# Kernel optimization log

Hardware: AMD Instinct MI355X
Metric: run time of the kernel (lower is better)

## Reference

```python
import jax, jax.numpy as jnp
import numpy as np

N_QUBITS = 8
DIM = 2 ** N_QUBITS  # 256
BSZ = 32768
N_OPS = 20

# Deterministic stand-in for tq.RandomLayer(n_ops=20): a fixed random list of
# {rx, ry, rz, cnot} ops on random wires, angles supplied via rl_angles.
_rng = np.random.RandomState(0)
_RL_OPS = []
for _i in range(N_OPS):
    _kind = ['rx', 'ry', 'rz', 'cnot'][int(_rng.randint(4))]
    if _kind == 'cnot':
        _w = _rng.choice(N_QUBITS, 2, replace=False)
        _RL_OPS.append((_kind, int(_w[0]), int(_w[1])))
    else:
        _RL_OPS.append((_kind, int(_rng.randint(N_QUBITS)), -1))


def _apply_1q(state, wire, kind, half_angle):
    """Apply a single-qubit rotation to state [bsz, DIM]. wire 0 = MSB."""
    bsz = state.shape[0]
    left = 2 ** wire
    right = DIM // (2 * left)
    st = state.reshape(bsz, left, 2, right)
    ha = jnp.broadcast_to(jnp.asarray(half_angle).reshape(-1), (bsz,))
    c = jnp.cos(ha)[:, None, None]
    s = jnp.sin(ha)[:, None, None]
    s0, s1 = st[:, :, 0, :], st[:, :, 1, :]
    if kind == 'ry':
        n0, n1 = c * s0 - s * s1, s * s0 + c * s1
    elif kind == 'rx':
        n0, n1 = c * s0 - 1j * s * s1, -1j * s * s0 + c * s1
    else:  # rz
        n0, n1 = (c - 1j * s) * s0, (c + 1j * s) * s1
    return jnp.stack([n0, n1], axis=2).reshape(bsz, DIM)


def _apply_cnot(state, control, target):
    bsz = state.shape[0]
    st = state.reshape((bsz,) + (2,) * N_QUBITS)
    c_ax, t_ax = 1 + control, 1 + target
    a = jnp.take(st, 0, axis=c_ax)  # control = 0 block: identity
    b = jnp.take(st, 1, axis=c_ax)  # control = 1 block: X on target
    b = jnp.flip(b, axis=t_ax - (1 if t_ax > c_ax else 0))
    return jnp.stack([a, b], axis=c_ax).reshape(bsz, DIM)


# Precomputed PauliZ sign table: signs[w, k] = +1 if bit w of k is 0 else -1.
_idx = np.arange(DIM)
_bits = (_idx[None, :] >> (N_QUBITS - 1 - np.arange(N_QUBITS)[:, None])) & 1
_SIGNS = jnp.asarray(1.0 - 2.0 * _bits, jnp.float32)  # [N_QUBITS, DIM]


def setup_inputs() -> dict:
    key = jax.random.key(0)
    k1, k2, k3, k4 = jax.random.split(key, 4)
    return {
        'x': jax.random.uniform(k1, (BSZ, N_QUBITS), dtype=jnp.float32),
        'rl_angles': jax.random.normal(k2, (N_OPS,), dtype=jnp.float32),
        'theta_rx': jax.random.normal(k3, (1,), dtype=jnp.float32),
        'theta_ry': jax.random.normal(k4, (1,), dtype=jnp.float32),
    }


def reference(x, rl_angles, theta_rx, theta_ry):
    bsz = x.shape[0]
    # |0...0> initial state
    state = jnp.zeros((bsz, DIM), jnp.complex64).at[:, 0].set(1.0)
    # GeneralEncoder: RY(x_i) on wire i (per-sample angles)
    for i in range(N_QUBITS):
        state = _apply_1q(state, i, 'ry', x[:, i] * 0.5)
    # RandomLayer: 20 fixed random ops
    for k, (kind, w0, w1) in enumerate(_RL_OPS):
        if kind == 'cnot':
            state = _apply_cnot(state, w0, w1)
        else:
            state = _apply_1q(state, w0, kind, rl_angles[k] * 0.5)
    # shared trainable RX then RY on every wire
    for w in range(N_QUBITS):
        state = _apply_1q(state, w, 'rx', theta_rx[0] * 0.5)
        state = _apply_1q(state, w, 'ry', theta_ry[0] * 0.5)
    # MeasureAll(PauliZ): <Z_w> = sum_k |amp_k|^2 * sign(bit_w(k))
    probs = state.real ** 2 + state.imag ** 2  # [bsz, DIM]
    return probs @ _SIGNS.T  # [bsz, N_QUBITS]
```

## Files before the change

### kernel.cpp

```cpp
#include <hip/hip_runtime.h>
#include <stdint.h>

#define NQ 8
#define DIM 256
#define BSZ 32768
#define NOPS 20
#define SPT 2

typedef float v2f __attribute__((ext_vector_type(2)));


struct COps { int kind[NOPS]; int w0[NOPS]; int w1[NOPS]; };

struct CMT {
  uint32_t mt[624]; int pos;
  constexpr CMT(uint32_t seed) : mt{}, pos(624) {
    for (int i = 0; i < 624; ++i) {
      mt[i] = seed;
      seed = 1812433253u * (seed ^ (seed >> 30)) + (uint32_t)(i + 1);
    }
  }
  constexpr uint32_t next32() {
    if (pos >= 624) {
      for (int i = 0; i < 624; ++i) {
        uint32_t y = (mt[i] & 0x80000000u) | (mt[(i + 1) % 624] & 0x7fffffffu);
        mt[i] = mt[(i + 397) % 624] ^ (y >> 1) ^ ((y & 1u) ? 0x9908b0dfu : 0u);
      }
      pos = 0;
    }
    uint32_t y = mt[pos++];
    y ^= y >> 11; y ^= (y << 7) & 0x9d2c5680u; y ^= (y << 15) & 0xefc60000u; y ^= y >> 18;
    return y;
  }
  constexpr uint32_t interval(uint32_t mx) {
    if (mx == 0u) return 0u;
    uint32_t mask = mx;
    mask |= mask >> 1; mask |= mask >> 2; mask |= mask >> 4; mask |= mask >> 8; mask |= mask >> 16;
    uint32_t v = next32() & mask;
    while (v > mx) v = next32() & mask;
    return v;
  }
};

constexpr COps decode_ops() {
  COps o{}; CMT r(0u);
  for (int k = 0; k < NOPS; ++k) {
    const uint32_t kind = r.interval(3u);
    o.kind[k] = (int)kind;
    if (kind == 3u) {
      int perm[NQ] = {0,1,2,3,4,5,6,7};
      for (int i = NQ - 1; i >= 1; --i) {
        const uint32_t j = r.interval((uint32_t)i);
        const int t = perm[i]; perm[i] = perm[(int)j]; perm[(int)j] = t;
      }
      o.w0[k] = perm[0]; o.w1[k] = perm[1];
    } else {
      o.w0[k] = (int)r.interval(7u);
      o.w1[k] = -1;
    }
  }
  return o;
}

constexpr COps OPS = decode_ops();


__device__ __forceinline__ float rfl(float v) {
  return __builtin_bit_cast(float, __builtin_amdgcn_readfirstlane(__builtin_bit_cast(int, v)));
}

template<int MASK>
__device__ __forceinline__ float lanexf(float v) {
  int i = __builtin_bit_cast(int, v);
  int r;
  if constexpr (MASK == 1)      r = __builtin_amdgcn_update_dpp(0, i, 0xB1, 0xF, 0xF, true);
  else if constexpr (MASK == 2) r = __builtin_amdgcn_update_dpp(0, i, 0x4E, 0xF, 0xF, true);
  else if constexpr (MASK == 8) r = __builtin_amdgcn_update_dpp(0, i, 0x128, 0xF, 0xF, true);
  else {
    int h = __builtin_amdgcn_update_dpp(0, i, 0x141, 0xF, 0xF, true);
    r     = __builtin_amdgcn_update_dpp(0, h, 0x1B, 0xF, 0xF, true);
  }
  return __builtin_bit_cast(float, r);
}

template<int MASK>
__device__ __forceinline__ v2f lanex2(v2f v) {
  v2f r; r.x = lanexf<MASK>(v.x); r.y = lanexf<MASK>(v.y); return r;
}

__device__ __forceinline__ v2f vswap(v2f v) { return __builtin_shufflevector(v, v, 1, 0); }
__device__ __forceinline__ v2f vsplat(float s) { v2f r = {s, s}; return r; }


template<int W>
__device__ __forceinline__ void g_rx_t(v2f (&v)[16], int l, float t) {
  constexpr int m = 1 << (7 - W);
  const v2f tpm = {t, -t};
  if constexpr (m >= 16) {
    constexpr int M = m >> 4;
    #pragma unroll
    for (int j0 = 0; j0 < 16; ++j0) if ((j0 & M) == 0) {
      const int j1 = j0 | M;
      v2f a = v[j0], b = v[j1];
      v[j0] = a + tpm * vswap(b);
      v[j1] = b + tpm * vswap(a);
    }
  } else {
    #pragma unroll
    for (int j = 0; j < 16; ++j) {
      v2f x = lanex2<m>(v[j]);
      v[j] = v[j] + tpm * vswap(x);
    }
  }
}

template<int W>
__device__ __forceinline__ void g_ry_t(v2f (&v)[16], int l, float t) {
  constexpr int m = 1 << (7 - W);
  if constexpr (m >= 16) {
    constexpr int M = m >> 4;
    const v2f vtn = vsplat(-t), vtp = vsplat(t);
    #pragma unroll
    for (int j0 = 0; j0 < 16; ++j0) if ((j0 & M) == 0) {
      const int j1 = j0 | M;
      v2f a = v[j0], b = v[j1];
      v[j0] = a + vtn * b;
      v[j1] = b + vtp * a;
    }
  } else {
    const v2f ts = vsplat((l & m) ? t : -t);
    #pragma unroll
    for (int j = 0; j < 16; ++j) {
      v2f x = lanex2<m>(v[j]);
      v[j] = v[j] + ts * x;
    }
  }
}

template<int W>
__device__ __forceinline__ void g_rz_t(v2f (&v)[16], int l, float t) {
  constexpr int m = 1 << (7 - W);
  if constexpr (m >= 16) {
    constexpr int M = m >> 4;
    const v2f tpm = {t, -t};
    #pragma unroll
    for (int j = 0; j < 16; ++j) {
      v2f sw = vswap(v[j]);
      if ((j & M) == 0) v[j] = v[j] + tpm * sw;
      else              v[j] = v[j] - tpm * sw;
    }
  } else {
    const v2f ts = (l & m) ? (v2f){-t, t} : (v2f){t, -t};
    #pragma unroll
    for (int j = 0; j < 16; ++j) v[j] = v[j] + ts * vswap(v[j]);
  }
}

template<int WC, int WT>
__device__ __forceinline__ void g_cnot(v2f (&v)[16], int l) {
  constexpr int mc = 1 << (7 - WC);
  constexpr int mt = 1 << (7 - WT);
  if constexpr (mt >= 16) {
    constexpr int M = mt >> 4;
    if constexpr (mc >= 16) {
      constexpr int MC = mc >> 4;
      #pragma unroll
      for (int j0 = 0; j0 < 16; ++j0) if ((j0 & M) == 0 && (j0 & MC) != 0) {
        const int j1 = j0 | M;
        v2f t = v[j0]; v[j0] = v[j1]; v[j1] = t;
      }
    } else {
      const bool bit = (l & mc) != 0;
      #pragma unroll
      for (int j0 = 0; j0 < 16; ++j0) if ((j0 & M) == 0) {
        const int j1 = j0 | M;
        v2f a = v[j0], b = v[j1];
        v[j0] = bit ? b : a;
        v[j1] = bit ? a : b;
      }
    }
  } else {
    if constexpr (mc >= 16) {
      constexpr int MC = mc >> 4;
      #pragma unroll
      for (int j = 0; j < 16; ++j) if (j & MC) v[j] = lanex2<mt>(v[j]);
    } else if constexpr ((mc == 8 || mc == 4) && mt != 4) {
      constexpr int BM   = (mc == 8) ? 0xC : 0xA;
      constexpr int ctrl = (mt == 1) ? 0xB1 : (mt == 2) ? 0x4E : 0x128;
      #pragma unroll
      for (int j = 0; j < 16; ++j) {
        int ir = __builtin_bit_cast(int, v[j].x);
        int ii = __builtin_bit_cast(int, v[j].y);
        ir = __builtin_amdgcn_update_dpp(ir, ir, ctrl, 0xF, BM, false);
        ii = __builtin_amdgcn_update_dpp(ii, ii, ctrl, 0xF, BM, false);
        v[j].x = __builtin_bit_cast(float, ir);
        v[j].y = __builtin_bit_cast(float, ii);
      }
    } else {
      const bool bit = (l & mc) != 0;
      #pragma unroll
      for (int j = 0; j < 16; ++j) {
        v2f x = lanex2<mt>(v[j]);
        v[j] = bit ? x : v[j];
      }
    }
  }
}

template<int K>
__device__ __forceinline__ void compute_t(const float* __restrict__ rl, float (&tv)[NOPS], float& cacc) {
  if constexpr (K < NOPS) {
    if constexpr (OPS.kind[K] != 3) {
      float sn, cs;
      __sincosf(0.5f * rl[K], &sn, &cs);
      tv[K] = rfl(sn * __builtin_amdgcn_rcpf(cs));
      cacc *= cs;
    }
    compute_t<K + 1>(rl, tv, cacc);
  }
}

template<int K>
__device__ __forceinline__ void apply_ops(v2f (&v)[16], int l, const float (&tv)[NOPS]) {
  if constexpr (K < NOPS) {
    constexpr int kind = OPS.kind[K];
    if constexpr (kind == 3)      g_cnot<OPS.w0[K], OPS.w1[K]>(v, l);
    else if constexpr (kind == 0) g_rx_t<OPS.w0[K]>(v, l, tv[K]);
    else if constexpr (kind == 1) g_ry_t<OPS.w0[K]>(v, l, tv[K]);
    else                          g_rz_t<OPS.w0[K]>(v, l, tv[K]);
    apply_ops<K + 1>(v, l, tv);
  }
}


template<int M>
__device__ __forceinline__ float xy_inlane(const v2f (&v)[16], float tnx, float tny) {
  v2f aRe = {0.f, 0.f}, aIm = {0.f, 0.f};
  #pragma unroll
  for (int j0 = 0; j0 < 16; ++j0) if ((j0 & M) == 0) {
    const int j1 = j0 | M;
    aRe += v[j0] * v[j1];
    aIm += v[j0] * vswap(v[j1]);
  }
  return tnx * (aRe.x + aRe.y) + tny * (aIm.x - aIm.y);
}

template<int MASK>
__device__ __forceinline__ float xy_cross(const v2f (&v)[16], int l, float nx, float ny) {
  v2f aRe = {0.f, 0.f}, aIm = {0.f, 0.f};
  #pragma unroll
  for (int j = 0; j < 16; ++j) {
    v2f x = lanex2<MASK>(v[j]);
    aRe += v[j] * x;
    aIm += v[j] * vswap(x);
  }
  const float nys = (l & MASK) ? -ny : ny;
  return nx * (aRe.x + aRe.y) + nys * (aIm.x - aIm.y);
}

__device__ __forceinline__ void init_state(v2f (&v)[16], const float* __restrict__ xrow, int l) {
  const float4* xp = reinterpret_cast<const float4*>(xrow);
  const float4 xa = xp[0], xb = xp[1];
  float sw[8], cw[8];
  __sincosf(0.5f * xa.x, &sw[0], &cw[0]);
  __sincosf(0.5f * xa.y, &sw[1], &cw[1]);
  __sincosf(0.5f * xa.z, &sw[2], &cw[2]);
  __sincosf(0.5f * xa.w, &sw[3], &cw[3]);
  __sincosf(0.5f * xb.x, &sw[4], &cw[4]);
  __sincosf(0.5f * xb.y, &sw[5], &cw[5]);
  __sincosf(0.5f * xb.z, &sw[6], &cw[6]);
  __sincosf(0.5f * xb.w, &sw[7], &cw[7]);

  const float pl = ((l & 8) ? sw[4] : cw[4]) * ((l & 4) ? sw[5] : cw[5]) *
                   ((l & 2) ? sw[6] : cw[6]) * ((l & 1) ? sw[7] : cw[7]);
  const float p01[4] = {cw[0]*cw[1], cw[0]*sw[1], sw[0]*cw[1], sw[0]*sw[1]};
  const float p23[4] = {cw[2]*cw[3], cw[2]*sw[3], sw[2]*cw[3], sw[2]*sw[3]};
  const float p01l[4] = {p01[0]*pl, p01[1]*pl, p01[2]*pl, p01[3]*pl};
  #pragma unroll
  for (int j = 0; j < 16; ++j) { v[j].x = p01l[j >> 2] * p23[j & 3]; v[j].y = 0.f; }
}

__global__ __launch_bounds__(256)
void qcnn_kernel(const float* __restrict__ x, const float* __restrict__ rl,
                 const float* __restrict__ thx, const float* __restrict__ thy,
                 float* __restrict__ out)
{
  const int tid = blockIdx.x * blockDim.x + threadIdx.x;
  const int p = tid >> 4;
  const int l = tid & 15;

  float tv[NOPS];
  float cacc = 1.0f;
  compute_t<0>(rl, tv, cacc);
  const float C2 = cacc * cacc;

  float sxf, cxf, syf, cyf;
  __sincosf(thx[0], &sxf, &cxf);
  __sincosf(thy[0], &syf, &cyf);
  const float nx = -syf * C2, ny = cyf * sxf * C2, nz = cyf * cxf * C2;
  const float tnx = 2.f * nx, tny = 2.f * ny;

  #pragma unroll 1
  for (int it = 0; it < SPT; ++it) {
    const int b = p * SPT + it;

    v2f v[16];
    init_state(v, x + (size_t)b * 8, l);
    apply_ops<0>(v, l, tv);

    v2f P2 = {0,0}, A0v = {0,0}, A1v = {0,0}, A2v = {0,0}, A3v = {0,0};
    #pragma unroll
    for (int j = 0; j < 16; ++j) {
      const v2f q = v[j] * v[j];
      P2 += q;
      if (j & 8) A0v -= q; else A0v += q;
      if (j & 4) A1v -= q; else A1v += q;
      if (j & 2) A2v -= q; else A2v += q;
      if (j & 1) A3v -= q; else A3v += q;
    }
    const float P  = P2.x + P2.y;
    const float A0 = A0v.x + A0v.y, A1 = A1v.x + A1v.y;
    const float A2 = A2v.x + A2v.y, A3 = A3v.x + A3v.y;

    float t0 = fmaf(nz, A0, xy_inlane<8>(v, tnx, tny));
    float t1 = fmaf(nz, A1, xy_inlane<4>(v, tnx, tny));
    float t2 = fmaf(nz, A2, xy_inlane<2>(v, tnx, tny));
    float t3 = fmaf(nz, A3, xy_inlane<1>(v, tnx, tny));
    float t4 = fmaf(nz, (l & 8) ? -P : P, xy_cross<8>(v, l, nx, ny));
    float t5 = fmaf(nz, (l & 4) ? -P : P, xy_cross<4>(v, l, nx, ny));
    float t6 = fmaf(nz, (l & 2) ? -P : P, xy_cross<2>(v, l, nx, ny));
    float t7 = fmaf(nz, (l & 1) ? -P : P, xy_cross<1>(v, l, nx, ny));

    #define RED_STEP(MK) \
      t0 += lanexf<MK>(t0); t1 += lanexf<MK>(t1); t2 += lanexf<MK>(t2); t3 += lanexf<MK>(t3); \
      t4 += lanexf<MK>(t4); t5 += lanexf<MK>(t5); t6 += lanexf<MK>(t6); t7 += lanexf<MK>(t7);
    RED_STEP(1) RED_STEP(2) RED_STEP(4) RED_STEP(8)
    #undef RED_STEP

    if (l == 0) {
      float4* o = reinterpret_cast<float4*>(out + (size_t)b * 8);
      const float4 o0 = {t0, t1, t2, t3};
      const float4 o1 = {t4, t5, t6, t7};
      o[0] = o0; o[1] = o1;
    }
  }
}


extern "C" void kernel_launch(void* const* d_in, const int* in_sizes, int n_in,
                              void* d_out, int out_size, void* d_ws, size_t ws_size,
                              hipStream_t stream) {
  const float* x   = (const float*)d_in[0];
  const float* rl  = (const float*)d_in[1];
  const float* thx = (const float*)d_in[2];
  const float* thy = (const float*)d_in[3];
  float* out = (float*)d_out;

  const int threads = 256;
  const int blocks = BSZ / (SPT * (threads / 16));
  qcnn_kernel<<<blocks, threads, 0, stream>>>(x, rl, thx, thy, out);
}
```

Measured before the change: 25.67 us.

## Precompute gate constants in a prep kernel and drop per-thread sample loop

Moves the per-thread sincos and reciprocal work for the 20 random-layer angles and the shared RX/RY measurement coefficients into a single-thread prep kernel that writes them to workspace. The main kernel then loads them as float4 values. It also removes the two-samples-per-thread loop, so each 16-lane group handles one sample and the grid doubles. The cost is an extra kernel launch and a serial dependency between the two kernels, in exchange for less redundant transcendental work in every thread.

```diff
diff --git a/kernel.cpp b/kernel.cpp
--- a/kernel.cpp
+++ b/kernel.cpp
@@ -5,7 +5,6 @@
 #define DIM 256
 #define BSZ 32768
 #define NOPS 20
-#define SPT 2
 
 typedef float v2f __attribute__((ext_vector_type(2)));
 
@@ -204,19 +203,6 @@
         v[j] = bit ? x : v[j];
       }
     }
-  }
-}
-
-template<int K>
-__device__ __forceinline__ void compute_t(const float* __restrict__ rl, float (&tv)[NOPS], float& cacc) {
-  if constexpr (K < NOPS) {
-    if constexpr (OPS.kind[K] != 3) {
-      float sn, cs;
-      __sincosf(0.5f * rl[K], &sn, &cs);
-      tv[K] = rfl(sn * __builtin_amdgcn_rcpf(cs));
-      cacc *= cs;
-    }
-    compute_t<K + 1>(rl, tv, cacc);
   }
 }
 
@@ -280,69 +266,85 @@
   for (int j = 0; j < 16; ++j) { v[j].x = p01l[j >> 2] * p23[j & 3]; v[j].y = 0.f; }
 }
 
+__global__ void prep_kernel(const float* __restrict__ rl, const float* __restrict__ thx,
+                            const float* __restrict__ thy, float* __restrict__ ws) {
+  if (threadIdx.x != 0 || blockIdx.x != 0) return;
+  float cacc = 1.f;
+  #pragma unroll
+  for (int k = 0; k < NOPS; ++k) {
+    float t = 0.f;
+    if (OPS.kind[k] != 3) {
+      float sn, cs; __sincosf(0.5f * rl[k], &sn, &cs);
+      t = sn / cs; cacc *= cs;
+    }
+    ws[k] = t;
+  }
+  const float C2 = cacc * cacc;
+  float sx, cx, sy, cy;
+  __sincosf(thx[0], &sx, &cx);
+  __sincosf(thy[0], &sy, &cy);
+  const float nx = -sy * C2, ny = cy * sx * C2, nz = cy * cx * C2;
+  ws[20] = nx; ws[21] = ny; ws[22] = nz; ws[23] = 2.f * nx; ws[24] = 2.f * ny;
+}
+
 __global__ __launch_bounds__(256)
-void qcnn_kernel(const float* __restrict__ x, const float* __restrict__ rl,
-                 const float* __restrict__ thx, const float* __restrict__ thy,
+void qcnn_kernel(const float* __restrict__ x, const float* __restrict__ ws,
                  float* __restrict__ out)
 {
   const int tid = blockIdx.x * blockDim.x + threadIdx.x;
-  const int p = tid >> 4;
+  const int b = tid >> 4;
   const int l = tid & 15;
 
+  const float4* wv = reinterpret_cast<const float4*>(ws);
+  const float4 q0 = wv[0], q1 = wv[1], q2 = wv[2], q3 = wv[3], q4 = wv[4], q5 = wv[5];
+  const float w24 = ws[24];
   float tv[NOPS];
-  float cacc = 1.0f;
-  compute_t<0>(rl, tv, cacc);
-  const float C2 = cacc * cacc;
-
-  float sxf, cxf, syf, cyf;
-  __sincosf(thx[0], &sxf, &cxf);
-  __sincosf(thy[0], &syf, &cyf);
-  const float nx = -syf * C2, ny = cyf * sxf * C2, nz = cyf * cxf * C2;
-  const float tnx = 2.f * nx, tny = 2.f * ny;
-
-  #pragma unroll 1
-  for (int it = 0; it < SPT; ++it) {
-    const int b = p * SPT + it;
-
-    v2f v[16];
-    init_state(v, x + (size_t)b * 8, l);
-    apply_ops<0>(v, l, tv);
-
-    v2f P2 = {0,0}, A0v = {0,0}, A1v = {0,0}, A2v = {0,0}, A3v = {0,0};
-    #pragma unroll
-    for (int j = 0; j < 16; ++j) {
-      const v2f q = v[j] * v[j];
-      P2 += q;
-      if (j & 8) A0v -= q; else A0v += q;
-      if (j & 4) A1v -= q; else A1v += q;
-      if (j & 2) A2v -= q; else A2v += q;
-      if (j & 1) A3v -= q; else A3v += q;
-    }
-    const float P  = P2.x + P2.y;
-    const float A0 = A0v.x + A0v.y, A1 = A1v.x + A1v.y;
-    const float A2 = A2v.x + A2v.y, A3 = A3v.x + A3v.y;
-
-    float t0 = fmaf(nz, A0, xy_inlane<8>(v, tnx, tny));
-    float t1 = fmaf(nz, A1, xy_inlane<4>(v, tnx, tny));
-    float t2 = fmaf(nz, A2, xy_inlane<2>(v, tnx, tny));
-    float t3 = fmaf(nz, A3, xy_inlane<1>(v, tnx, tny));
-    float t4 = fmaf(nz, (l & 8) ? -P : P, xy_cross<8>(v, l, nx, ny));
-    float t5 = fmaf(nz, (l & 4) ? -P : P, xy_cross<4>(v, l, nx, ny));
-    float t6 = fmaf(nz, (l & 2) ? -P : P, xy_cross<2>(v, l, nx, ny));
-    float t7 = fmaf(nz, (l & 1) ? -P : P, xy_cross<1>(v, l, nx, ny));
-
-    #define RED_STEP(MK) \
-      t0 += lanexf<MK>(t0); t1 += lanexf<MK>(t1); t2 += lanexf<MK>(t2); t3 += lanexf<MK>(t3); \
-      t4 += lanexf<MK>(t4); t5 += lanexf<MK>(t5); t6 += lanexf<MK>(t6); t7 += lanexf<MK>(t7);
-    RED_STEP(1) RED_STEP(2) RED_STEP(4) RED_STEP(8)
-    #undef RED_STEP
-
-    if (l == 0) {
-      float4* o = reinterpret_cast<float4*>(out + (size_t)b * 8);
-      const float4 o0 = {t0, t1, t2, t3};
-      const float4 o1 = {t4, t5, t6, t7};
-      o[0] = o0; o[1] = o1;
-    }
+  tv[0]=rfl(q0.x); tv[1]=rfl(q0.y); tv[2]=rfl(q0.z); tv[3]=rfl(q0.w);
+  tv[4]=rfl(q1.x); tv[5]=rfl(q1.y); tv[6]=rfl(q1.z); tv[7]=rfl(q1.w);
+  tv[8]=rfl(q2.x); tv[9]=rfl(q2.y); tv[10]=rfl(q2.z); tv[11]=rfl(q2.w);
+  tv[12]=rfl(q3.x); tv[13]=rfl(q3.y); tv[14]=rfl(q3.z); tv[15]=rfl(q3.w);
+  tv[16]=rfl(q4.x); tv[17]=rfl(q4.y); tv[18]=rfl(q4.z); tv[19]=rfl(q4.w);
+  const float nx = rfl(q5.x), ny = rfl(q5.y), nz = rfl(q5.z);
+  const float tnx = rfl(q5.w), tny = rfl(w24);
+
+  v2f v[16];
+  init_state(v, x + (size_t)b * 8, l);
+  apply_ops<0>(v, l, tv);
+
+  v2f P2 = {0,0}, A0v = {0,0}, A1v = {0,0}, A2v = {0,0}, A3v = {0,0};
+  #pragma unroll
+  for (int j = 0; j < 16; ++j) {
+    const v2f q = v[j] * v[j];
+    P2 += q;
+    if (j & 8) A0v -= q; else A0v += q;
+    if (j & 4) A1v -= q; else A1v += q;
+    if (j & 2) A2v -= q; else A2v += q;
+    if (j & 1) A3v -= q; else A3v += q;
+  }
+  const float P  = P2.x + P2.y;
+  const float A0 = A0v.x + A0v.y, A1 = A1v.x + A1v.y;
+  const float A2 = A2v.x + A2v.y, A3 = A3v.x + A3v.y;
+
+  float t0 = fmaf(nz, A0, xy_inlane<8>(v, tnx, tny));
+  float t1 = fmaf(nz, A1, xy_inlane<4>(v, tnx, tny));
+  float t2 = fmaf(nz, A2, xy_inlane<2>(v, tnx, tny));
+  float t3 = fmaf(nz, A3, xy_inlane<1>(v, tnx, tny));
+  float t4 = fmaf(nz, (l & 8) ? -P : P, xy_cross<8>(v, l, nx, ny));
+  float t5 = fmaf(nz, (l & 4) ? -P : P, xy_cross<4>(v, l, nx, ny));
+  float t6 = fmaf(nz, (l & 2) ? -P : P, xy_cross<2>(v, l, nx, ny));
+  float t7 = fmaf(nz, (l & 1) ? -P : P, xy_cross<1>(v, l, nx, ny));
+
+  #define RED_STEP(MK) \
+    t0 += lanexf<MK>(t0); t1 += lanexf<MK>(t1); t2 += lanexf<MK>(t2); t3 += lanexf<MK>(t3); \
+    t4 += lanexf<MK>(t4); t5 += lanexf<MK>(t5); t6 += lanexf<MK>(t6); t7 += lanexf<MK>(t7);
+  RED_STEP(1) RED_STEP(2) RED_STEP(4) RED_STEP(8)
+  #undef RED_STEP
+
+  if (l == 0) {
+    float4* o = reinterpret_cast<float4*>(out + (size_t)b * 8);
+    const float4 o0 = {t0, t1, t2, t3};
+    const float4 o1 = {t4, t5, t6, t7};
+    o[0] = o0; o[1] = o1;
   }
 }
 
@@ -355,8 +357,11 @@
   const float* thx = (const float*)d_in[2];
   const float* thy = (const float*)d_in[3];
   float* out = (float*)d_out;
+  float* ws  = (float*)d_ws;
+
+  prep_kernel<<<1, 64, 0, stream>>>(rl, thx, thy, ws);
 
   const int threads = 256;
-  const int blocks = BSZ / (SPT * (threads / 16));
-  qcnn_kernel<<<blocks, threads, 0, stream>>>(x, rl, thx, thy, out);
-}
+  const int blocks = BSZ / (threads / 16);
+  qcnn_kernel<<<blocks, threads, 0, stream>>>(x, ws, out);
+}
```

Measured after the change: 28.60 us. 1.11x slower.
